# Performance work log

Measured on AMD Instinct MI355X. Metric: run time of the kernel, lower is better.

## Reference

```python
import jax, jax.numpy as jnp
import numpy as np
import math

B, S, H = 4, 1024, 1024
E, TOP_K, WINDOW = 4, 2, 64
CONFIGS = [(8, 'standard'), (12, 'standard'), (8, 'linear'), (8, 'local')]
PARAM_NAMES = ['Wq', 'bq', 'Wk', 'bk', 'Wv', 'bv', 'Wo', 'bo']


def setup_inputs() -> dict:
    key = jax.random.key(0)
    ks = jax.random.split(key, 2 + 8 * E)
    d = {}
    d['x'] = jax.random.normal(ks[0], (B, S, H), jnp.float32)
    d['Wg'] = jax.random.normal(ks[1], (H, E), jnp.float32) * 0.02
    i = 2
    for e, (nh, _) in enumerate(CONFIGS):
        hd = H // nh
        pd = nh * hd  # 1020 for nh=12, else 1024
        shapes = [(H, pd), (pd,), (H, pd), (pd,), (H, pd), (pd,), (pd, H), (H,)]
        for nm, shp in zip(PARAM_NAMES, shapes):
            d[f'e{e}_{nm}'] = jax.random.normal(ks[i], shp, jnp.float32) * 0.02
            i += 1
    d['attention_mask'] = jnp.ones((B, S), jnp.int32)
    return d


def _heads(y, nh, hd):
    b, s, _ = y.shape
    return y.reshape(b, s, nh, hd).transpose(0, 2, 1, 3)  # [b, nh, s, hd]


def _attention_expert(x, mask, Wq, bq, Wk, bk, Wv, bv, Wo, bo, nh, atype):
    b, s, _ = x.shape
    hd = Wq.shape[1] // nh
    scale = math.sqrt(hd)
    q = _heads(x @ Wq + bq, nh, hd)
    k = _heads(x @ Wk + bk, nh, hd)
    v = _heads(x @ Wv + bv, nh, hd)
    if atype == 'linear':
        # kernel-trick linear attention; original ignores attention_mask here
        q = jax.nn.elu(q) + 1.0
        k = jax.nn.elu(k) + 1.0
        kv = jnp.einsum('bhsd,bhse->bhde', k, v)
        num = jnp.einsum('bhqd,bhde->bhqe', q, kv)
        den = jnp.einsum('bhqd,bhd->bhq', q, k.sum(axis=2)) + 1e-6
        out = num / den[..., None]
    else:
        scores = jnp.einsum('bhqd,bhkd->bhqk', q, k) / scale
        if atype == 'local':
            idx = jnp.arange(s)
            dist = idx[None, :] - idx[:, None]  # j - i
            local_mask = jnp.abs(dist) <= WINDOW // 2
            scores = jnp.where(local_mask[None, None], scores, -jnp.inf)
        scores = jnp.where(mask[:, None, None, :] == 0, -jnp.inf, scores)
        probs = jax.nn.softmax(scores, axis=-1)
        probs = jnp.where(jnp.isnan(probs), 0.0, probs)  # nan_to_num(nan=0)
        out = jnp.einsum('bhqk,bhkd->bhqd', probs, v)
    out = out.transpose(0, 2, 1, 3).reshape(b, s, -1)
    return out @ Wo + bo


def _forward(x, Wg, eparams, attention_mask):
    b, s, h = x.shape
    # TopKGating (eval mode: no noise). logits -> top_k -> softmax over selected
    logits = x.reshape(-1, h) @ Wg  # [b*s, E]
    top_vals, top_idx = jax.lax.top_k(logits, TOP_K)
    gate_w = jax.nn.softmax(top_vals, axis=-1).reshape(b, s, TOP_K)
    sel = top_idx.reshape(b, s, TOP_K)
    outs = jnp.stack([
        _attention_expert(x, attention_mask, *eparams[e], CONFIGS[e][0], CONFIGS[e][1])
        for e in range(E)
    ], axis=0)  # [E, b, s, h]
    perm = outs.transpose(1, 2, 0, 3)  # [b, s, E, h]
    selected = jnp.take_along_axis(perm, sel[..., None], axis=2)  # [b, s, K, h]
    return (selected * gate_w[..., None]).sum(axis=2)


def reference(x, Wg,
              e0_Wq, e0_bq, e0_Wk, e0_bk, e0_Wv, e0_bv, e0_Wo, e0_bo,
              e1_Wq, e1_bq, e1_Wk, e1_bk, e1_Wv, e1_bv, e1_Wo, e1_bo,
              e2_Wq, e2_bq, e2_Wk, e2_bk, e2_Wv, e2_bv, e2_Wo, e2_bo,
              e3_Wq, e3_bq, e3_Wk, e3_bk, e3_Wv, e3_bv, e3_Wo, e3_bo,
              attention_mask):
    eparams = [
        (e0_Wq, e0_bq, e0_Wk, e0_bk, e0_Wv, e0_bv, e0_Wo, e0_bo),
        (e1_Wq, e1_bq, e1_Wk, e1_bk, e1_Wv, e1_bv, e1_Wo, e1_bo),
        (e2_Wq, e2_bq, e2_Wk, e2_bk, e2_Wv, e2_bv, e2_Wo, e2_bo),
        (e3_Wq, e3_bq, e3_Wk, e3_bk, e3_Wv, e3_bv, e3_Wo, e3_bo),
    ]
    return _forward(x, Wg, eparams, attention_mask)
```

## Files before the change

### kernel.cpp

```cpp
#include <hip/hip_runtime.h>
#include <cmath>

#define B_ 4
#define S_ 1024
#define H_ 1024

typedef short bf16x8 __attribute__((ext_vector_type(8)));
typedef float f32x4 __attribute__((ext_vector_type(4)));
typedef _Float16 half4 __attribute__((ext_vector_type(4)));

__device__ __forceinline__ unsigned short f2bf(float f) {
  unsigned u = __float_as_uint(f);
  u += 0x7fff + ((u >> 16) & 1);
  return (unsigned short)(u >> 16);
}
__device__ __forceinline__ float bf2f(unsigned short h) {
  return __uint_as_float(((unsigned)h) << 16);
}
__device__ __forceinline__ void gld16(const void* g, void* l) {
  __builtin_amdgcn_global_load_lds(
      (const __attribute__((address_space(1))) unsigned int*)g,
      (__attribute__((address_space(3))) unsigned int*)l, 16, 0, 0);
}

__global__ __launch_bounds__(64) void gate_kernel(
    const float* __restrict__ x, const float* __restrict__ Wg,
    float* __restrict__ gw) {
  int t = blockIdx.x;
  int lane = threadIdx.x;
  const float* xr = x + (size_t)t * H_;
  float a0 = 0.f, a1 = 0.f, a2 = 0.f, a3 = 0.f;
  for (int h = lane; h < H_; h += 64) {
    float xv = xr[h];
    const float* wr = Wg + h * 4;
    a0 += xv * wr[0]; a1 += xv * wr[1]; a2 += xv * wr[2]; a3 += xv * wr[3];
  }
  for (int off = 32; off > 0; off >>= 1) {
    a0 += __shfl_down(a0, off);
    a1 += __shfl_down(a1, off);
    a2 += __shfl_down(a2, off);
    a3 += __shfl_down(a3, off);
  }
  if (lane == 0) {
    float v[4] = {a0, a1, a2, a3};
    int i0 = 0; float b0 = v[0];
    for (int e = 1; e < 4; ++e) if (v[e] > b0) { b0 = v[e]; i0 = e; }
    int i1 = -1; float b1 = -INFINITY;
    for (int e = 0; e < 4; ++e) { if (e == i0) continue; if (v[e] > b1) { b1 = v[e]; i1 = e; } }
    float e1v = expf(b1 - b0);
    float w0 = 1.f / (1.f + e1v);
    float w1 = e1v / (1.f + e1v);
    float o[4] = {0.f, 0.f, 0.f, 0.f};
    o[i0] = w0; o[i1] = w1;
    float* g = gw + t * 4;
    g[0] = o[0]; g[1] = o[1]; g[2] = o[2]; g[3] = o[3];
  }
}

__global__ __launch_bounds__(64) void gate_conv_kernel(
    const float* __restrict__ x, const float* __restrict__ Wg,
    float* __restrict__ gw, unsigned short* __restrict__ xb) {
  int t = blockIdx.x;
  int lane = threadIdx.x;
  const float* xr = x + (size_t)t * H_;
  unsigned short* xbr = xb + (size_t)t * H_;
  float a0 = 0.f, a1 = 0.f, a2 = 0.f, a3 = 0.f;
  for (int h = lane; h < H_; h += 64) {
    float xv = xr[h];
    xbr[h] = f2bf(xv);
    const float* wr = Wg + h * 4;
    a0 += xv * wr[0]; a1 += xv * wr[1]; a2 += xv * wr[2]; a3 += xv * wr[3];
  }
  for (int off = 32; off > 0; off >>= 1) {
    a0 += __shfl_down(a0, off);
    a1 += __shfl_down(a1, off);
    a2 += __shfl_down(a2, off);
    a3 += __shfl_down(a3, off);
  }
  if (lane == 0) {
    float v[4] = {a0, a1, a2, a3};
    int i0 = 0; float b0 = v[0];
    for (int e = 1; e < 4; ++e) if (v[e] > b0) { b0 = v[e]; i0 = e; }
    int i1 = -1; float b1 = -INFINITY;
    for (int e = 0; e < 4; ++e) { if (e == i0) continue; if (v[e] > b1) { b1 = v[e]; i1 = e; } }
    float e1v = expf(b1 - b0);
    float w0 = 1.f / (1.f + e1v);
    float w1 = e1v / (1.f + e1v);
    float o[4] = {0.f, 0.f, 0.f, 0.f};
    o[i0] = w0; o[i1] = w1;
    float* g = gw + t * 4;
    g[0] = o[0]; g[1] = o[1]; g[2] = o[2]; g[3] = o[3];
  }
}

__global__ __launch_bounds__(256) void conv_kernel(
    const float* __restrict__ src, unsigned short* __restrict__ dst,
    int nsrc, int ldsrc) {
  int idx = blockIdx.x * 256 + threadIdx.x;
  int m = idx >> 10, c = idx & 1023;
  dst[idx] = (c < nsrc) ? f2bf(src[(size_t)m * ldsrc + c]) : (unsigned short)0;
}

__global__ __launch_bounds__(256) void wtrans4_kernel(
    const float* __restrict__ s0, const float* __restrict__ s1,
    const float* __restrict__ s2, const float* __restrict__ s3,
    unsigned short* __restrict__ d0, unsigned short* __restrict__ d1,
    unsigned short* __restrict__ d2, unsigned short* __restrict__ d3, int pd) {
  __shared__ float tile[32][33];
  int z = blockIdx.z;
  const float* src = (z == 0) ? s0 : (z == 1) ? s1 : (z == 2) ? s2 : s3;
  unsigned short* dst = (z == 0) ? d0 : (z == 1) ? d1 : (z == 2) ? d2 : d3;
  int ksrc = (z < 3) ? 1024 : pd;
  int nsrc = (z < 3) ? pd : 1024;
  int ldsrc = (z < 3) ? pd : 1024;
  int k0 = blockIdx.x * 32, n0 = blockIdx.y * 32;
  int tx = threadIdx.x & 31, ty = threadIdx.x >> 5;
  for (int i = 0; i < 32; i += 8) {
    int k = k0 + ty + i, n = n0 + tx;
    tile[ty + i][tx] = (k < ksrc && n < nsrc) ? src[(size_t)k * ldsrc + n] : 0.f;
  }
  __syncthreads();
  for (int i = 0; i < 32; i += 8) {
    int n = n0 + ty + i, k = k0 + tx;
    dst[(size_t)n * 1024 + k] = f2bf(tile[tx][ty + i]);
  }
}

struct W16 {
  const float* src[16];
  unsigned short* dst[16];
  int pd[4];
};
__global__ __launch_bounds__(256) void wtrans16_kernel(W16 p) {
  __shared__ float tile[32][33];
  int z = blockIdx.z;
  int e = z >> 2, m = z & 3;
  const float* src = p.src[z];
  unsigned short* dst = p.dst[z];
  int pd = p.pd[e];
  int ksrc = (m < 3) ? 1024 : pd;
  int nsrc = (m < 3) ? pd : 1024;
  int ldsrc = (m < 3) ? pd : 1024;
  int k0 = blockIdx.x * 32, n0 = blockIdx.y * 32;
  int tx = threadIdx.x & 31, ty = threadIdx.x >> 5;
  for (int i = 0; i < 32; i += 8) {
    int k = k0 + ty + i, n = n0 + tx;
    tile[ty + i][tx] = (k < ksrc && n < nsrc) ? src[(size_t)k * ldsrc + n] : 0.f;
  }
  __syncthreads();
  for (int i = 0; i < 32; i += 8) {
    int n = n0 + ty + i, k = k0 + tx;
    dst[(size_t)n * 1024 + k] = f2bf(tile[tx][ty + i]);
  }
}

__global__ __launch_bounds__(256) void gemm_mfma(
    const unsigned short* __restrict__ A, const unsigned short* __restrict__ Bt,
    const float* __restrict__ b0, const float* __restrict__ b1,
    const float* __restrict__ b2, void* __restrict__ Cv, int ldc,
    int nact, int elu_ncut, int out_bf16, int mode,
    const float* __restrict__ gw, int expert, int remap,
    int qs_ncut, float qscale) {
  constexpr int K = 1024;
  __shared__ __align__(16) unsigned short As[128 * 32];
  __shared__ __align__(16) unsigned short Bs[128 * 32];
  int tid = threadIdx.x, wave = tid >> 6, lane = tid & 63;
  int quad = lane >> 4, lrow = lane & 15;
  int rw = (wave >> 1) * 64, cw = (wave & 1) * 64;
  int m0 = blockIdx.y * 128, n0 = blockIdx.x * 128;
  int srow = wave * 32 + (lane >> 2);
  int scol = (lane & 3) * 8;
  const unsigned short* gA = A + (size_t)(m0 + srow) * K + scol;
  const unsigned short* gB = Bt + (size_t)(n0 + srow) * K + scol;
  unsigned short* lA = &As[wave * 1024];
  unsigned short* lB = &Bs[wave * 1024];
  f32x4 acc[4][4];
#pragma unroll
  for (int mt = 0; mt < 4; ++mt)
#pragma unroll
    for (int nt = 0; nt < 4; ++nt) acc[mt][nt] = (f32x4){0.f, 0.f, 0.f, 0.f};

  for (int k0 = 0; k0 < K; k0 += 32) {
    gld16(gA + k0, lA);
    gld16(gA + 16 * K + k0, lA + 512);
    gld16(gB + k0, lB);
    gld16(gB + 16 * K + k0, lB + 512);
    __syncthreads();
    bf16x8 af[4], bfr[4];
#pragma unroll
    for (int t = 0; t < 4; ++t) {
      af[t]  = *(const bf16x8*)&As[(rw + t * 16 + lrow) * 32 + quad * 8];
      bfr[t] = *(const bf16x8*)&Bs[(cw + t * 16 + lrow) * 32 + quad * 8];
    }
#pragma unroll
    for (int mt = 0; mt < 4; ++mt)
#pragma unroll
      for (int nt = 0; nt < 4; ++nt)
        acc[mt][nt] = __builtin_amdgcn_mfma_f32_16x16x32_bf16(
            af[mt], bfr[nt], acc[mt][nt], 0, 0, 0);
    __syncthreads();
  }
#pragma unroll
  for (int nt = 0; nt < 4; ++nt) {
    int n = n0 + cw + nt * 16 + lrow;
    int slice = n >> 10, noff = n & 1023;
    if (noff >= nact) continue;
    const float* bp = (slice == 0) ? b0 : (slice == 1) ? b1 : b2;
    float bias = bp[noff];
    bool do_elu = n < elu_ncut;
    bool do_qs = n < qs_ncut;
    int col = n;
    if (remap) {
      int head = (noff * 12337) >> 20;
      col = slice * 1152 + head * 96 + (noff - head * 85);
    }
#pragma unroll
    for (int mt = 0; mt < 4; ++mt) {
      int mb = m0 + rw + mt * 16 + quad * 4;
#pragma unroll
      for (int r = 0; r < 4; ++r) {
        int m = mb + r;
        float val = acc[mt][nt][r] + bias;
        if (do_elu) val = (val > 0.f) ? val + 1.f : expf(val);
        if (do_qs) val *= qscale;
        size_t ci = (size_t)m * ldc + col;
        if (out_bf16) {
          ((unsigned short*)Cv)[ci] = f2bf(val);
        } else {
          float* C = (float*)Cv;
          if (mode == 0) C[ci] = val;
          else {
            float g = gw[m * 4 + expert];
            if (mode == 1) C[ci] = g * val;
            else           C[ci] += g * val;
          }
        }
      }
    }
  }
}

struct QkvP {
  const unsigned short* Bt[4];
  const float* bq[4];
  const float* bk[4];
  const float* bv[4];
  unsigned short* C[4];
  int ldc[4];
  int nact[4];
  int elu_ncut[4];
  int remap[4];
  int qs_ncut[4];
  float qscale[4];
};
__global__ __launch_bounds__(256) void gemm_qkv4(
    const unsigned short* __restrict__ A, QkvP p) {
  constexpr int K = 1024;
  __shared__ __align__(16) unsigned short As[2 * 128 * 32];
  __shared__ __align__(16) unsigned short Bs[2 * 128 * 32];
  int e = blockIdx.z;
  const unsigned short* Bt = p.Bt[e];
  unsigned short* Cv = p.C[e];
  int ldc = p.ldc[e], nact = p.nact[e], elu_ncut = p.elu_ncut[e];
  int remap = p.remap[e], qs_ncut = p.qs_ncut[e];
  float qscale = p.qscale[e];
  int tid = threadIdx.x, wave = tid >> 6, lane = tid & 63;
  int quad = lane >> 4, lrow = lane & 15;
  int rw = (wave >> 1) * 64, cw = (wave & 1) * 64;
  int m0 = blockIdx.y * 128, n0 = blockIdx.x * 128;
  int srow = wave * 32 + (lane >> 2);
  int scol = (lane & 3) * 8;
  const unsigned short* gA = A + (size_t)(m0 + srow) * K + scol;
  const unsigned short* gB = Bt + (size_t)(n0 + srow) * K + scol;
  unsigned short* lA = &As[wave * 1024];
  unsigned short* lB = &Bs[wave * 1024];
  f32x4 acc[4][4];
#pragma unroll
  for (int mt = 0; mt < 4; ++mt)
#pragma unroll
    for (int nt = 0; nt < 4; ++nt) acc[mt][nt] = (f32x4){0.f, 0.f, 0.f, 0.f};

  for (int k0 = 0; k0 < K; k0 += 64) {
    gld16(gA + k0, lA);
    gld16(gA + 16 * K + k0, lA + 512);
    gld16(gA + k0 + 32, lA + 4096);
    gld16(gA + 16 * K + k0 + 32, lA + 4096 + 512);
    gld16(gB + k0, lB);
    gld16(gB + 16 * K + k0, lB + 512);
    gld16(gB + k0 + 32, lB + 4096);
    gld16(gB + 16 * K + k0 + 32, lB + 4096 + 512);
    __syncthreads();
#pragma unroll
    for (int kk = 0; kk < 2; ++kk) {
      const unsigned short* Ap = As + kk * 4096;
      const unsigned short* Bp = Bs + kk * 4096;
      bf16x8 af[4], bfr[4];
#pragma unroll
      for (int t = 0; t < 4; ++t) {
        af[t]  = *(const bf16x8*)&Ap[(rw + t * 16 + lrow) * 32 + quad * 8];
        bfr[t] = *(const bf16x8*)&Bp[(cw + t * 16 + lrow) * 32 + quad * 8];
      }
#pragma unroll
      for (int mt = 0; mt < 4; ++mt)
#pragma unroll
        for (int nt = 0; nt < 4; ++nt)
          acc[mt][nt] = __builtin_amdgcn_mfma_f32_16x16x32_bf16(
              af[mt], bfr[nt], acc[mt][nt], 0, 0, 0);
    }
    __syncthreads();
  }
#pragma unroll
  for (int nt = 0; nt < 4; ++nt) {
    int n = n0 + cw + nt * 16 + lrow;
    int slice = n >> 10, noff = n & 1023;
    if (noff >= nact) continue;
    const float* bp = (slice == 0) ? p.bq[e] : (slice == 1) ? p.bk[e] : p.bv[e];
    float bias = bp[noff];
    bool do_elu = n < elu_ncut;
    bool do_qs = n < qs_ncut;
    int col = n;
    if (remap) {
      int head = (noff * 12337) >> 20;
      col = slice * 1152 + head * 96 + (noff - head * 85);
    }
#pragma unroll
    for (int mt = 0; mt < 4; ++mt) {
      int mb = m0 + rw + mt * 16 + quad * 4;
#pragma unroll
      for (int r = 0; r < 4; ++r) {
        int m = mb + r;
        float val = acc[mt][nt][r] + bias;
        if (do_elu) val = (val > 0.f) ? val + 1.f : expf(val);
        if (do_qs) val *= qscale;
        Cv[(size_t)m * ldc + col] = f2bf(val);
      }
    }
  }
}

struct OutP {
  const unsigned short* A[4];
  const unsigned short* B[4];
  const float* bias[4];
};

__global__ __launch_bounds__(256) void gemm_out4(
    OutP p, const float* __restrict__ gw, float* __restrict__ part) {
  constexpr int K = 1024;
  __shared__ __align__(16) unsigned short As[2 * 128 * 32];
  __shared__ __align__(16) unsigned short Bs[2 * 128 * 32];
  int e = blockIdx.z;
  const unsigned short* A = p.A[e];
  const unsigned short* Bt = p.B[e];
  const float* bp = p.bias[e];
  float* C = part + (size_t)e * (4096ull * 1024ull);
  int tid = threadIdx.x, wave = tid >> 6, lane = tid & 63;
  int quad = lane >> 4, lrow = lane & 15;
  int rw = (wave >> 1) * 64, cw = (wave & 1) * 64;
  int m0 = blockIdx.y * 128, n0 = blockIdx.x * 128;
  int srow = wave * 32 + (lane >> 2);
  int scol = (lane & 3) * 8;
  const unsigned short* gA = A + (size_t)(m0 + srow) * K + scol;
  const unsigned short* gB = Bt + (size_t)(n0 + srow) * K + scol;
  unsigned short* lA = &As[wave * 1024];
  unsigned short* lB = &Bs[wave * 1024];
  f32x4 acc[4][4];
#pragma unroll
  for (int mt = 0; mt < 4; ++mt)
#pragma unroll
    for (int nt = 0; nt < 4; ++nt) acc[mt][nt] = (f32x4){0.f, 0.f, 0.f, 0.f};

  for (int k0 = 0; k0 < K; k0 += 64) {
    gld16(gA + k0, lA);
    gld16(gA + 16 * K + k0, lA + 512);
    gld16(gA + k0 + 32, lA + 4096);
    gld16(gA + 16 * K + k0 + 32, lA + 4096 + 512);
    gld16(gB + k0, lB);
    gld16(gB + 16 * K + k0, lB + 512);
    gld16(gB + k0 + 32, lB + 4096);
    gld16(gB + 16 * K + k0 + 32, lB + 4096 + 512);
    __syncthreads();
#pragma unroll
    for (int kk = 0; kk < 2; ++kk) {
      const unsigned short* Ap = As + kk * 4096;
      const unsigned short* Bp = Bs + kk * 4096;
      bf16x8 af[4], bfr[4];
#pragma unroll
      for (int t = 0; t < 4; ++t) {
        af[t]  = *(const bf16x8*)&Ap[(rw + t * 16 + lrow) * 32 + quad * 8];
        bfr[t] = *(const bf16x8*)&Bp[(cw + t * 16 + lrow) * 32 + quad * 8];
      }
#pragma unroll
      for (int mt = 0; mt < 4; ++mt)
#pragma unroll
        for (int nt = 0; nt < 4; ++nt)
          acc[mt][nt] = __builtin_amdgcn_mfma_f32_16x16x32_bf16(
              af[mt], bfr[nt], acc[mt][nt], 0, 0, 0);
    }
    __syncthreads();
  }
#pragma unroll
  for (int nt = 0; nt < 4; ++nt) {
    int n = n0 + cw + nt * 16 + lrow;
    float bias = bp[n];
#pragma unroll
    for (int mt = 0; mt < 4; ++mt) {
      int mb = m0 + rw + mt * 16 + quad * 4;
#pragma unroll
      for (int r = 0; r < 4; ++r) {
        int m = mb + r;
        float g = gw[m * 4 + e];
        C[(size_t)m * 1024 + n] = g * (acc[mt][nt][r] + bias);
      }
    }
  }
}

__global__ __launch_bounds__(256) void reduce4(
    const float* __restrict__ part, float* __restrict__ out) {
  constexpr size_t N = 4096ull * 1024ull;
  size_t idx = ((size_t)blockIdx.x * 256 + threadIdx.x) * 4;
  f32x4 a0 = *(const f32x4*)(part + idx);
  f32x4 a1 = *(const f32x4*)(part + idx + N);
  f32x4 a2 = *(const f32x4*)(part + idx + 2 * N);
  f32x4 a3 = *(const f32x4*)(part + idx + 3 * N);
  f32x4 s;
#pragma unroll
  for (int j = 0; j < 4; ++j) {
    float t = a0[j];
    t += a1[j]; t += a2[j]; t += a3[j];
    s[j] = t;
  }
  *(f32x4*)(out + idx) = s;
}

__global__ __launch_bounds__(256) void padzero(
    unsigned short* __restrict__ qkv1, unsigned short* __restrict__ aob1) {
  int idx = blockIdx.x * 256 + threadIdx.x;
  int m = idx / 396, r = idx % 396;
  int slice = r / 132, r2 = r % 132;
  int head = r2 / 11, c = 85 + r2 % 11;
  qkv1[(size_t)m * 3456 + slice * 1152 + head * 96 + c] = 0;
  if (idx < 4096 * 4) {
    int mm = idx >> 2, cc = 1020 + (idx & 3);
    aob1[(size_t)mm * 1024 + cc] = 0;
  }
}

template <int HD, bool LOCAL>
__device__ __forceinline__ void attn_body(
    char* smem,
    const unsigned short* __restrict__ q, const unsigned short* __restrict__ k,
    const unsigned short* __restrict__ v, const int* __restrict__ amask,
    unsigned short* __restrict__ ao, int ldq, int h) {
  constexpr int HDP = (HD + 31) & ~31;
  constexpr int DCH = HDP / 32;
  constexpr int NDT = HDP / 16;
  constexpr int NCH = HDP / 8;
  constexpr int QT = 256, KT = 64;
  constexpr int KLD = HDP + 8;
  constexpr int VLD = KT + 4;
  constexpr int W2 = 32;
  constexpr int KSZ = KT * KLD;
  constexpr int VSZ = HDP * VLD;
  unsigned short* Ks = (unsigned short*)smem;
  _Float16* Vt = (_Float16*)(smem + 2 * KSZ * 2);
  unsigned long long* amq =
      (unsigned long long*)(smem + 2 * KSZ * 2 + 2 * VSZ * 2);
  int tid = threadIdx.x, wave = tid >> 6, lane = tid & 63;
  int quad = lane >> 4, l15 = lane & 15;
  int q0 = blockIdx.x * QT, b = blockIdx.z;
  size_t baseq = ((size_t)b * S_) * ldq + (size_t)h * HDP;
  size_t baseo = ((size_t)b * S_) * H_ + (size_t)h * HD;

  {
    unsigned long long bb0 = __ballot(amask[b * S_ + wave * 128 + lane] != 0);
    unsigned long long bb1 = __ballot(amask[b * S_ + wave * 128 + 64 + lane] != 0);
    if (lane == 0) { amq[wave * 2] = bb0; amq[wave * 2 + 1] = bb1; }
  }

  int qrow[2];
  bf16x8 qf[2][DCH];
#pragma unroll
  for (int g = 0; g < 2; ++g) {
    qrow[g] = q0 + wave * 32 + g * 16 + l15;
#pragma unroll
    for (int c = 0; c < DCH; ++c)
#pragma unroll
      for (int j = 0; j < 8; ++j) {
        int d = c * 32 + quad * 8 + j;
        qf[g][c][j] =
            (d < HD) ? (short)q[baseq + (size_t)qrow[g] * ldq + d] : (short)0;
      }
  }

  int jlo = 0, jhi = S_;
  if (LOCAL) {
    jlo = q0 - W2; if (jlo < 0) jlo = 0; jlo &= ~(KT - 1);
    jhi = q0 + QT + W2; if (jhi > S_) jhi = S_;
  }

  int skey = tid & 63, sc8a = tid >> 6, sc8b = 8 + (tid >> 6);
  bool sactb = sc8b < NCH;
  const unsigned short* kg = k + baseq + (size_t)skey * ldq;
  const unsigned short* vg = v + baseq + (size_t)skey * ldq;
  bf16x8 kra = {}, krb = {}, vra = {}, vrb = {};
  {
    size_t o = (size_t)jlo * ldq;
    kra = *(const bf16x8*)(kg + o + sc8a * 8);
    vra = *(const bf16x8*)(vg + o + sc8a * 8);
    if (sactb) {
      krb = *(const bf16x8*)(kg + o + sc8b * 8);
      vrb = *(const bf16x8*)(vg + o + sc8b * 8);
    }
  }

  {
    *(bf16x8*)&Ks[skey * KLD + sc8a * 8] = kra;
#pragma unroll
    for (int j = 0; j < 8; ++j)
      Vt[(sc8a * 8 + j) * VLD + skey] = (_Float16)bf2f((unsigned short)vra[j]);
    if (sactb) {
      *(bf16x8*)&Ks[skey * KLD + sc8b * 8] = krb;
#pragma unroll
      for (int j = 0; j < 8; ++j)
        Vt[(sc8b * 8 + j) * VLD + skey] = (_Float16)bf2f((unsigned short)vrb[j]);
    }
  }
  int cur = 0;
  __syncthreads();

  float m_run[2] = {-1e30f, -1e30f}, l_run[2] = {0.f, 0.f};
  f32x4 accd[2][NDT];
#pragma unroll
  for (int g = 0; g < 2; ++g)
#pragma unroll
    for (int dt = 0; dt < NDT; ++dt) accd[g][dt] = (f32x4){0.f, 0.f, 0.f, 0.f};

  for (int j0 = jlo; j0 < jhi; j0 += KT) {
    int jn = j0 + KT;
    if (jn < jhi) {
      size_t o = (size_t)jn * ldq;
      kra = *(const bf16x8*)(kg + o + sc8a * 8);
      vra = *(const bf16x8*)(vg + o + sc8a * 8);
      if (sactb) {
        krb = *(const bf16x8*)(kg + o + sc8b * 8);
        vrb = *(const bf16x8*)(vg + o + sc8b * 8);
      }
    }
    const unsigned short* KsR = Ks + cur * KSZ;
    const _Float16* VtR = Vt + cur * VSZ;
    f32x4 sf[2][4];
#pragma unroll
    for (int kt = 0; kt < 4; ++kt) {
      sf[0][kt] = (f32x4){0.f, 0.f, 0.f, 0.f};
      sf[1][kt] = (f32x4){0.f, 0.f, 0.f, 0.f};
#pragma unroll
      for (int c = 0; c < DCH; ++c) {
        bf16x8 kf = *(const bf16x8*)&KsR[(kt * 16 + l15) * KLD + c * 32 + quad * 8];
        sf[0][kt] = __builtin_amdgcn_mfma_f32_16x16x32_bf16(kf, qf[0][c], sf[0][kt], 0, 0, 0);
        sf[1][kt] = __builtin_amdgcn_mfma_f32_16x16x32_bf16(kf, qf[1][c], sf[1][kt], 0, 0, 0);
      }
    }
    unsigned long long mb = amq[j0 >> 6];
    unsigned mw[2] = {(unsigned)mb, (unsigned)(mb >> 32)};
    float pvv[2][4][4];
    float mx[2] = {-1e30f, -1e30f};
#pragma unroll
    for (int kt = 0; kt < 4; ++kt) {
      unsigned word = mw[kt >> 1];
      int sh = (kt & 1) * 16 + quad * 4;
#pragma unroll
      for (int r = 0; r < 4; ++r) {
        bool okm = (word >> (sh + r)) & 1;
#pragma unroll
        for (int g = 0; g < 2; ++g) {
          bool ok = okm;
          if (LOCAL) {
            int dj = (j0 + kt * 16 + quad * 4 + r) - qrow[g];
            ok = ok && (dj <= W2) && (dj >= -W2);
          }
          float s = ok ? sf[g][kt][r] : -1e30f;
          pvv[g][kt][r] = s;
          mx[g] = fmaxf(mx[g], s);
        }
      }
    }
    half4 pf[2][4];
    float aR[2][4];
#pragma unroll
    for (int g = 0; g < 2; ++g) {
      float mxg = fmaxf(mx[g], __shfl_xor(mx[g], 16));
      mxg = fmaxf(mxg, __shfl_xor(mxg, 32));
      float m_new = fmaxf(m_run[g], mxg);
      float psum = 0.f;
#pragma unroll
      for (int kt = 0; kt < 4; ++kt)
#pragma unroll
        for (int r = 0; r < 4; ++r) {
          float s = pvv[g][kt][r];
          float p = (s > -1e29f) ? __builtin_amdgcn_exp2f(s - m_new) : 0.f;
          pvv[g][kt][r] = p;
          psum += p;
        }
      psum += __shfl_xor(psum, 16);
      psum += __shfl_xor(psum, 32);
      float alpha = __builtin_amdgcn_exp2f(m_run[g] - m_new);
      m_run[g] = m_new;
      l_run[g] = l_run[g] * alpha + psum;
#pragma unroll
      for (int r = 0; r < 4; ++r)
        aR[g][r] = __shfl(alpha, (lane & 48) | (quad * 4 + r));
#pragma unroll
      for (int dt = 0; dt < NDT; ++dt)
#pragma unroll
        for (int r = 0; r < 4; ++r) accd[g][dt][r] *= aR[g][r];
#pragma unroll
      for (int kt = 0; kt < 4; ++kt)
#pragma unroll
        for (int r = 0; r < 4; ++r) pf[g][kt][r] = (_Float16)pvv[g][kt][r];
    }
    if (jn < jhi) {
      unsigned short* KsW = Ks + (cur ^ 1) * KSZ;
      _Float16* VtW = Vt + (cur ^ 1) * VSZ;
      *(bf16x8*)&KsW[skey * KLD + sc8a * 8] = kra;
#pragma unroll
      for (int j = 0; j < 8; ++j)
        VtW[(sc8a * 8 + j) * VLD + skey] = (_Float16)bf2f((unsigned short)vra[j]);
      if (sactb) {
        *(bf16x8*)&KsW[skey * KLD + sc8b * 8] = krb;
#pragma unroll
        for (int j = 0; j < 8; ++j)
          VtW[(sc8b * 8 + j) * VLD + skey] = (_Float16)bf2f((unsigned short)vrb[j]);
      }
    }
#pragma unroll
    for (int dt = 0; dt < NDT; ++dt)
#pragma unroll
      for (int kt = 0; kt < 4; ++kt) {
        half4 vf = *(const half4*)&VtR[(dt * 16 + l15) * VLD + kt * 16 + quad * 4];
        accd[0][dt] = __builtin_amdgcn_mfma_f32_16x16x16f16(pf[0][kt], vf, accd[0][dt], 0, 0, 0);
        accd[1][dt] = __builtin_amdgcn_mfma_f32_16x16x16f16(pf[1][kt], vf, accd[1][dt], 0, 0, 0);
      }
    __syncthreads();
    cur ^= 1;
  }
#pragma unroll
  for (int g = 0; g < 2; ++g) {
    float linv = (l_run[g] > 0.f) ? 1.f / l_run[g] : 0.f;
    float lR[4];
#pragma unroll
    for (int r = 0; r < 4; ++r)
      lR[r] = __shfl(linv, (lane & 48) | (quad * 4 + r));
#pragma unroll
    for (int dt = 0; dt < NDT; ++dt) {
      int d = dt * 16 + l15;
      if (d >= HD) continue;
#pragma unroll
      for (int r = 0; r < 4; ++r) {
        int row = q0 + wave * 32 + g * 16 + quad * 4 + r;
        ao[baseo + (size_t)row * H_ + d] = f2bf(accd[g][dt][r] * lR[r]);
      }
    }
  }
}

template <int HD, bool LOCAL>
__global__ __launch_bounds__(512) void attn_mfma3(
    const unsigned short* __restrict__ q, const unsigned short* __restrict__ k,
    const unsigned short* __restrict__ v, const int* __restrict__ amask,
    unsigned short* __restrict__ ao, int ldq) {
  constexpr int HDP = (HD + 31) & ~31;
  __shared__ __align__(16) char smem[2 * 64 * (HDP + 8) * 2 + 2 * HDP * 68 * 2 + 128];
  attn_body<HD, LOCAL>(smem, q, k, v, amask, ao, ldq, blockIdx.y);
}

#define NSPLIT 4
__device__ __forceinline__ void linkv_body(
    char* smemi, const unsigned short* __restrict__ k,
    const unsigned short* __restrict__ v, float* __restrict__ kvp,
    float* __restrict__ ksump, int ld, int h, int b, int split, int tid) {
  constexpr int HD = 128;
  constexpr int TLD = 34;
  unsigned short* Kt = (unsigned short*)smemi;
  unsigned short* Vt = Kt + HD * TLD;
  int bh = b * 8 + h;
  int wave = tid >> 6, lane = tid & 63;
  int quad = lane >> 4, l15 = lane & 15;
  int rw = (wave >> 1) * 64, cw = (wave & 1) * 64;
  size_t base = ((size_t)b * S_) * ld + (size_t)h * HD;
  int s_begin = split * (S_ / NSPLIT);

  f32x4 acc[4][4];
#pragma unroll
  for (int mt = 0; mt < 4; ++mt)
#pragma unroll
    for (int nt = 0; nt < 4; ++nt) acc[mt][nt] = (f32x4){0.f, 0.f, 0.f, 0.f};
  float ksacc = 0.f;
  int myd = tid & 127, half = tid >> 7;

  for (int c0 = 0; c0 < S_ / NSPLIT; c0 += 32) {
    for (int idx = tid; idx < 32 * HD; idx += 256) {
      int d = idx & 127, s = idx >> 7;
      size_t g = base + (size_t)(s_begin + c0 + s) * ld + d;
      Kt[d * TLD + s] = k[g];
      Vt[d * TLD + s] = v[g];
    }
    __syncthreads();
    bf16x8 af[4], bf[4];
#pragma unroll
    for (int t = 0; t < 4; ++t) {
      af[t] = *(const bf16x8*)&Vt[(rw + t * 16 + l15) * TLD + quad * 8];
      bf[t] = *(const bf16x8*)&Kt[(cw + t * 16 + l15) * TLD + quad * 8];
    }
#pragma unroll
    for (int mt = 0; mt < 4; ++mt)
#pragma unroll
      for (int nt = 0; nt < 4; ++nt)
        acc[mt][nt] = __builtin_amdgcn_mfma_f32_16x16x32_bf16(
            af[mt], bf[nt], acc[mt][nt], 0, 0, 0);
#pragma unroll
    for (int s = 0; s < 16; ++s)
      ksacc += bf2f(Kt[myd * TLD + half * 16 + s]);
    __syncthreads();
  }
  float* red = (float*)Kt;
  if (half == 1) red[myd] = ksacc;
  __syncthreads();
  if (half == 0)
    ksump[((size_t)split * 32 + bh) * HD + myd] = ksacc + red[myd];
  float* kvo = kvp + ((size_t)split * 32 + bh) * (HD * HD);
#pragma unroll
  for (int mt = 0; mt < 4; ++mt)
#pragma unroll
    for (int nt = 0; nt < 4; ++nt) {
      int dk = cw + nt * 16 + l15;
#pragma unroll
      for (int r = 0; r < 4; ++r) {
        int dv = rw + mt * 16 + quad * 4 + r;
        kvo[(size_t)dv * HD + dk] = acc[mt][nt][r];
      }
    }
}

__global__ __launch_bounds__(256) void linkv_mfma(
    const unsigned short* __restrict__ k, const unsigned short* __restrict__ v,
    float* __restrict__ kvp, float* __restrict__ ksump, int ld) {
  __shared__ __align__(16) char smemi[17408];
  linkv_body(smemi, k, v, kvp, ksump, ld, blockIdx.x, blockIdx.y, blockIdx.z,
             threadIdx.x);
}

__global__ __launch_bounds__(512) void attn_mega(
    const unsigned short* __restrict__ qkv0,
    const unsigned short* __restrict__ qkv1,
    const unsigned short* __restrict__ qkv2,
    const unsigned short* __restrict__ qkv3, const int* __restrict__ amask,
    unsigned short* __restrict__ ao0, unsigned short* __restrict__ ao1,
    unsigned short* __restrict__ ao3,
    float* __restrict__ kvp, float* __restrict__ ksump) {
  __shared__ __align__(16) char smem[69760];
  int y = blockIdx.y;
  if (y < 8)
    attn_body<128, false>(smem, qkv0, qkv0 + 1024, qkv0 + 2048, amask, ao0,
                          3072, y);
  else if (y < 20)
    attn_body<85, false>(smem, qkv1, qkv1 + 1152, qkv1 + 2304, amask, ao1,
                         3456, y - 8);
  else if (y < 28)
    attn_body<128, true>(smem, qkv3, qkv3 + 1024, qkv3 + 2048, amask, ao3,
                         3072, y - 20);
  else {
    int sub = threadIdx.x >> 8, stid = threadIdx.x & 255;
    int idx = (y - 28) * 8 + blockIdx.x * 2 + sub;
    linkv_body(smem + sub * 17408, qkv2 + 1024, qkv2 + 2048, kvp, ksump, 3072,
               idx & 7, blockIdx.z, idx >> 3, stid);
  }
}

__global__ __launch_bounds__(256) void linkv_reduce(
    const float* __restrict__ kvp, const float* __restrict__ ksump,
    unsigned short* __restrict__ kvb, float* __restrict__ ksum) {
  int idx = blockIdx.x * 256 + threadIdx.x;
  float s = 0.f;
#pragma unroll
  for (int p = 0; p < NSPLIT; ++p) s += kvp[(size_t)p * (32 * 128 * 128) + idx];
  kvb[idx] = f2bf(s);
  if (idx < 32 * 128) {
    float t = 0.f;
#pragma unroll
    for (int p = 0; p < NSPLIT; ++p) t += ksump[(size_t)p * (32 * 128) + idx];
    ksum[idx] = t;
  }
}

__global__ __launch_bounds__(256) void linattn_mfma(
    const unsigned short* __restrict__ q, const unsigned short* __restrict__ kvT,
    const float* __restrict__ ksum, unsigned short* __restrict__ ao, int ldq) {
  constexpr int KLD = 136;
  __shared__ __align__(16) unsigned short Ks[128 * KLD];
  __shared__ float ksL[128];
  int tid = threadIdx.x, wave = tid >> 6, lane = tid & 63;
  int quad = lane >> 4, l15 = lane & 15;
  int rw = (wave >> 1) * 64, cw = (wave & 1) * 64;
  int q0 = blockIdx.x * 128, h = blockIdx.y, b = blockIdx.z;
  int bh = b * 8 + h;
  size_t baseq = ((size_t)b * S_) * ldq + (size_t)h * 128;
  size_t baseo = ((size_t)b * S_) * H_ + (size_t)h * 128;
  const unsigned short* kvg = kvT + (size_t)bh * (128 * 128);
  for (int idx = tid; idx < 128 * 16; idx += 256) {
    int e = idx >> 4, c = idx & 15;
    *(bf16x8*)&Ks[e * KLD + c * 8] = *(const bf16x8*)&kvg[e * 128 + c * 8];
  }
  if (tid < 128) ksL[tid] = ksum[(size_t)bh * 128 + tid];
  bf16x8 qf[4][4];
#pragma unroll
  for (int mt = 0; mt < 4; ++mt) {
    const unsigned short* qr = q + baseq + (size_t)(q0 + rw + mt * 16 + l15) * ldq;
#pragma unroll
    for (int kc = 0; kc < 4; ++kc)
      qf[mt][kc] = *(const bf16x8*)&qr[kc * 32 + quad * 8];
  }
  __syncthreads();
  f32x4 acc[4][4];
#pragma unroll
  for (int mt = 0; mt < 4; ++mt)
#pragma unroll
    for (int nt = 0; nt < 4; ++nt) acc[mt][nt] = (f32x4){0.f, 0.f, 0.f, 0.f};
#pragma unroll
  for (int kc = 0; kc < 4; ++kc) {
    bf16x8 bf[4];
#pragma unroll
    for (int nt = 0; nt < 4; ++nt)
      bf[nt] = *(const bf16x8*)&Ks[(cw + nt * 16 + l15) * KLD + kc * 32 + quad * 8];
#pragma unroll
    for (int mt = 0; mt < 4; ++mt)
#pragma unroll
      for (int nt = 0; nt < 4; ++nt)
        acc[mt][nt] = __builtin_amdgcn_mfma_f32_16x16x32_bf16(
            qf[mt][kc], bf[nt], acc[mt][nt], 0, 0, 0);
  }
  float den[4];
#pragma unroll
  for (int mt = 0; mt < 4; ++mt) {
    float s = 0.f;
#pragma unroll
    for (int kc = 0; kc < 4; ++kc)
#pragma unroll
      for (int j = 0; j < 8; ++j)
        s += bf2f((unsigned short)qf[mt][kc][j]) * ksL[kc * 32 + quad * 8 + j];
    s += __shfl_xor(s, 16);
    s += __shfl_xor(s, 32);
    den[mt] = s;
  }
#pragma unroll
  for (int mt = 0; mt < 4; ++mt)
#pragma unroll
    for (int r = 0; r < 4; ++r) {
      float dv = __shfl(den[mt], (lane & 48) | (quad * 4 + r));
      float inv = 1.f / (dv + 1e-6f);
      int row = q0 + rw + mt * 16 + quad * 4 + r;
#pragma unroll
      for (int nt = 0; nt < 4; ++nt) {
        int col = cw + nt * 16 + l15;
        ao[baseo + (size_t)row * H_ + col] = f2bf(acc[mt][nt][r] * inv);
      }
    }
}

extern "C" void kernel_launch(void* const* d_in, const int* in_sizes, int n_in,
                              void* d_out, int out_size, void* d_ws, size_t ws_size,
                              hipStream_t stream) {
  const float* x = (const float*)d_in[0];
  const float* Wg = (const float*)d_in[1];
  const int* amask = (const int*)d_in[34];
  float* out = (float*)d_out;
  char* ws = (char*)d_ws;
  const size_t MiB = 1ull << 20;
  const int nhs[4] = {8, 12, 8, 8};
  const float LOG2E = 1.4426950408889634f;

  if (ws_size >= 157 * MiB) {
    float* gw = (float*)ws;
    float* ksum = (float*)(ws + (64ull << 10));
    unsigned short* kvb = (unsigned short*)(ws + 1 * MiB);
    unsigned short* xb = (unsigned short*)(ws + 4 * MiB);
    float* kvp = (float*)(ws + 4 * MiB);
    float* ksump = (float*)(ws + 12 * MiB);
    unsigned short* woT[4];
    for (int e = 0; e < 4; ++e)
      woT[e] = (unsigned short*)(ws + (18 + 2 * e) * MiB);
    const size_t qkvOff[4] = {26 * MiB, 50 * MiB, 77 * MiB, 101 * MiB};
    unsigned short* qkvE[4];
    for (int e = 0; e < 4; ++e) qkvE[e] = (unsigned short*)(ws + qkvOff[e]);
    float* part = (float*)(ws + 26 * MiB);
    unsigned short* aobE[4];
    for (int e = 0; e < 4; ++e)
      aobE[e] = (unsigned short*)(ws + (125 + 8 * e) * MiB);
    unsigned short* qkvT4 = (unsigned short*)(ws + 125 * MiB);

    gate_conv_kernel<<<4096, 64, 0, stream>>>(x, Wg, gw, xb);

    W16 w;
    for (int e = 0; e < 4; ++e) {
      w.pd[e] = nhs[e] * (H_ / nhs[e]);
      for (int m = 0; m < 3; ++m) {
        w.src[e * 4 + m] = (const float*)d_in[2 + 8 * e + 2 * m];
        w.dst[e * 4 + m] = qkvT4 + (size_t)(e * 3 + m) * (1 << 20);
      }
      w.src[e * 4 + 3] = (const float*)d_in[2 + 8 * e + 6];
      w.dst[e * 4 + 3] = woT[e];
    }
    wtrans16_kernel<<<dim3(32, 32, 16), 256, 0, stream>>>(w);

    QkvP qp;
    for (int e = 0; e < 4; ++e) {
      int hd = H_ / nhs[e];
      int pd = nhs[e] * hd;
      qp.Bt[e] = qkvT4 + (size_t)(e * 3) * (1 << 20);
      qp.bq[e] = (const float*)d_in[2 + 8 * e + 1];
      qp.bk[e] = (const float*)d_in[2 + 8 * e + 3];
      qp.bv[e] = (const float*)d_in[2 + 8 * e + 5];
      qp.C[e] = qkvE[e];
      qp.ldc[e] = (e == 1) ? 3456 : 3072;
      qp.nact[e] = (pd == 1020) ? 1020 : 1024;
      qp.elu_ncut[e] = (e == 2) ? 2048 : 0;
      qp.remap[e] = (e == 1) ? 1 : 0;
      qp.qs_ncut[e] = (e == 2) ? 0 : 1024;
      qp.qscale[e] = LOG2E / sqrtf((float)hd);
    }
    gemm_qkv4<<<dim3(24, 32, 4), 256, 0, stream>>>(xb, qp);

    padzero<<<6336, 256, 0, stream>>>(qkvE[1], aobE[1]);

    attn_mega<<<dim3(S_ / 256, 32, B_), 512, 0, stream>>>(
        qkvE[0], qkvE[1], qkvE[2], qkvE[3], amask, aobE[0], aobE[1], aobE[3],
        kvp, ksump);

    linkv_reduce<<<(32 * 128 * 128) / 256, 256, 0, stream>>>(kvp, ksump, kvb, ksum);
    linattn_mfma<<<dim3(S_ / 128, 8, B_), 256, 0, stream>>>(
        qkvE[2], kvb, ksum, aobE[2], 3072);

    OutP p;
    for (int e = 0; e < 4; ++e) {
      p.A[e] = aobE[e];
      p.B[e] = woT[e];
      p.bias[e] = (const float*)d_in[2 + 8 * e + 7];
    }
    gemm_out4<<<dim3(8, 32, 4), 256, 0, stream>>>(p, gw, part);
    reduce4<<<4096, 256, 0, stream>>>(part, out);
    return;
  }

  float* gw            = (float*)(ws + 0);
  unsigned short* kvb  = (unsigned short*)(ws + (1ull << 20));
  float* ksum          = (float*)(ws + (3ull << 20) + (1ull << 19));
  unsigned short* xb   = (unsigned short*)(ws + (4ull << 20));
  unsigned short* qkvT = (unsigned short*)(ws + (12ull << 20));
  unsigned short* woT  = (unsigned short*)(ws + (18ull << 20));
  unsigned short* qkv  = (unsigned short*)(ws + (20ull << 20));
  unsigned short* aob  = (unsigned short*)(ws + (49ull << 20));
  float* kvp           = (float*)(ws + (57ull << 20));
  float* ksump         = (float*)(ws + (73ull << 20));

  conv_kernel<<<16384, 256, 0, stream>>>(x, xb, 1024, 1024);
  gate_kernel<<<4096, 64, 0, stream>>>(x, Wg, gw);

  for (int e = 0; e < 4; ++e) {
    const float* Wq = (const float*)d_in[2 + 8 * e + 0];
    const float* bq = (const float*)d_in[2 + 8 * e + 1];
    const float* Wk = (const float*)d_in[2 + 8 * e + 2];
    const float* bk = (const float*)d_in[2 + 8 * e + 3];
    const float* Wv = (const float*)d_in[2 + 8 * e + 4];
    const float* bv = (const float*)d_in[2 + 8 * e + 5];
    const float* Wo = (const float*)d_in[2 + 8 * e + 6];
    const float* bo = (const float*)d_in[2 + 8 * e + 7];
    int nh = nhs[e];
    int hd = H_ / nh;
    int pd = nh * hd;
    int ldqkv = (e == 1) ? 3456 : 3072;
    int qs_ncut = (e == 2) ? 0 : 1024;
    float qscale = LOG2E / sqrtf((float)hd);

    wtrans4_kernel<<<dim3(32, 32, 4), 256, 0, stream>>>(
        Wq, Wk, Wv, Wo, qkvT, qkvT + (1 << 20), qkvT + (2 << 20), woT, pd);

    gemm_mfma<<<dim3(24, 32), 256, 0, stream>>>(
        xb, qkvT, bq, bk, bv, qkv, ldqkv,
        (pd == 1020) ? 1020 : 1024, (e == 2) ? 2048 : 0, 1, 0, nullptr, 0,
        (e == 1) ? 1 : 0, qs_ncut, qscale);

    if (e == 2) {
      const unsigned short* qb = qkv;
      const unsigned short* kb = qkv + 1024;
      const unsigned short* vb = qkv + 2048;
      linkv_mfma<<<dim3(8, B_, NSPLIT), 256, 0, stream>>>(kb, vb, kvp, ksump, 3072);
      linkv_reduce<<<(32 * 128 * 128) / 256, 256, 0, stream>>>(kvp, ksump, kvb, ksum);
      linattn_mfma<<<dim3(S_ / 128, 8, B_), 256, 0, stream>>>(qb, kvb, ksum, aob, 3072);
    } else if (e == 1) {
      attn_mfma3<85, false><<<dim3(S_ / 256, 12, B_), 512, 0, stream>>>(
          qkv, qkv + 1152, qkv + 2304, amask, aob, 3456);
    } else if (e == 3) {
      attn_mfma3<128, true><<<dim3(S_ / 256, 8, B_), 512, 0, stream>>>(
          qkv, qkv + 1024, qkv + 2048, amask, aob, 3072);
    } else {
      attn_mfma3<128, false><<<dim3(S_ / 256, 8, B_), 512, 0, stream>>>(
          qkv, qkv + 1024, qkv + 2048, amask, aob, 3072);
    }

    gemm_mfma<<<dim3(8, 32), 256, 0, stream>>>(
        aob, woT, bo, bo, bo, out, 1024, 1024, 0, 0, (e == 0) ? 1 : 2, gw, e, 0,
        0, 1.0f);
  }
}
```

Baseline: 527.8 us.

## Rewrite QKV and output GEMMs as 256x256 double-buffered tiles with swizzled LDS

```diff
diff --git a/kernel.cpp b/kernel.cpp
--- a/kernel.cpp
+++ b/kernel.cpp
@@ -240,6 +240,86 @@
   }
 }
 
+__device__ __forceinline__ void stage_half(
+    const unsigned short* __restrict__ G, int grow0, int kbase,
+    unsigned short* lhalf, int wave, int lane) {
+#pragma unroll
+  for (int j = 0; j < 2; ++j) {
+    int t = j * 512 + wave * 64 + lane;
+    int rl = t >> 3;
+    int cs = (t & 7) * 8;
+    int c0 = cs ^ (((rl >> 2) & 1) << 4);
+    gld16(G + (size_t)(grow0 + rl) * 1024 + kbase + c0,
+          lhalf + (size_t)(j * 512 + wave * 64) * 8);
+  }
+}
+
+__device__ __forceinline__ void gemm256_core(
+    const unsigned short* __restrict__ A, const unsigned short* __restrict__ Bt,
+    int m0, int n0, unsigned short* As, unsigned short* Bs,
+    f32x4 (&acc)[8][4]) {
+  int tid = threadIdx.x;
+  int wave = tid >> 6, lane = tid & 63;
+  int quad = lane >> 4, l15 = lane & 15;
+  int wr = wave >> 2, wc = wave & 3;
+#pragma unroll
+  for (int mr = 0; mr < 8; ++mr)
+#pragma unroll
+    for (int nr = 0; nr < 4; ++nr) acc[mr][nr] = (f32x4){0.f, 0.f, 0.f, 0.f};
+  stage_half(A, m0, 0, As, wave, lane);
+  stage_half(A, m0 + 128, 0, As + 8192, wave, lane);
+  stage_half(Bt, n0, 0, Bs, wave, lane);
+  stage_half(Bt, n0 + 128, 0, Bs + 8192, wave, lane);
+  __syncthreads();
+  int cur = 0;
+  for (int t = 0; t < 16; ++t) {
+    const unsigned short* Ar = As + cur * 16384;
+    const unsigned short* Br = Bs + cur * 16384;
+    unsigned short* Awr = As + (cur ^ 1) * 16384;
+    unsigned short* Bwr = Bs + (cur ^ 1) * 16384;
+    int kb = (t + 1) * 64;
+    bool more = (t + 1 < 16);
+    bf16x8 bfr[4];
+#pragma unroll
+    for (int p = 0; p < 4; ++p) {
+      const int ks = p >> 1, mh = (p & 1) * 4;
+      bf16x8 af[4];
+#pragma unroll
+      for (int i = 0; i < 4; ++i) {
+        int row = wr * 128 + (mh + i) * 16 + l15;
+        int c = ks * 32 + quad * 8;
+        af[i] = *(const bf16x8*)&Ar[row * 64 + (c ^ (((row >> 2) & 1) << 4))];
+      }
+      if ((p & 1) == 0) {
+#pragma unroll
+        for (int i = 0; i < 4; ++i) {
+          int row = wc * 64 + i * 16 + l15;
+          int c = ks * 32 + quad * 8;
+          bfr[i] = *(const bf16x8*)&Br[row * 64 + (c ^ (((row >> 2) & 1) << 4))];
+        }
+      }
+      if (more) {
+        if (p == 0) stage_half(A, m0, kb, Awr, wave, lane);
+        else if (p == 1) stage_half(A, m0 + 128, kb, Awr + 8192, wave, lane);
+        else if (p == 2) stage_half(Bt, n0, kb, Bwr, wave, lane);
+        else stage_half(Bt, n0 + 128, kb, Bwr + 8192, wave, lane);
+      }
+      __builtin_amdgcn_s_barrier();
+      __builtin_amdgcn_s_setprio(1);
+#pragma unroll
+      for (int i = 0; i < 4; ++i)
+#pragma unroll
+        for (int jn = 0; jn < 4; ++jn)
+          acc[mh + i][jn] = __builtin_amdgcn_mfma_f32_16x16x32_bf16(
+              af[i], bfr[jn], acc[mh + i][jn], 0, 0, 0);
+      __builtin_amdgcn_s_setprio(0);
+      __builtin_amdgcn_s_barrier();
+    }
+    __syncthreads();
+    cur ^= 1;
+  }
+}
+
 struct QkvP {
   const unsigned short* Bt[4];
   const float* bq[4];
@@ -253,65 +333,26 @@
   int qs_ncut[4];
   float qscale[4];
 };
-__global__ __launch_bounds__(256) void gemm_qkv4(
+__global__ __launch_bounds__(512, 1) void gemm_qkv4_v2(
     const unsigned short* __restrict__ A, QkvP p) {
-  constexpr int K = 1024;
-  __shared__ __align__(16) unsigned short As[2 * 128 * 32];
-  __shared__ __align__(16) unsigned short Bs[2 * 128 * 32];
+  __shared__ __align__(16) unsigned short As[2 * 256 * 64];
+  __shared__ __align__(16) unsigned short Bs[2 * 256 * 64];
   int e = blockIdx.z;
-  const unsigned short* Bt = p.Bt[e];
+  int flat = blockIdx.y * 12 + blockIdx.x;
+  int swz = (flat & 7) * 24 + (flat >> 3);
+  int m0 = (swz / 12) * 256, n0 = (swz % 12) * 256;
+  f32x4 acc[8][4];
+  gemm256_core(A, p.Bt[e], m0, n0, As, Bs, acc);
+  int nact = p.nact[e], elu_ncut = p.elu_ncut[e], remap = p.remap[e];
+  int qs_ncut = p.qs_ncut[e], ldc = p.ldc[e];
+  float qscale = p.qscale[e];
   unsigned short* Cv = p.C[e];
-  int ldc = p.ldc[e], nact = p.nact[e], elu_ncut = p.elu_ncut[e];
-  int remap = p.remap[e], qs_ncut = p.qs_ncut[e];
-  float qscale = p.qscale[e];
   int tid = threadIdx.x, wave = tid >> 6, lane = tid & 63;
-  int quad = lane >> 4, lrow = lane & 15;
-  int rw = (wave >> 1) * 64, cw = (wave & 1) * 64;
-  int m0 = blockIdx.y * 128, n0 = blockIdx.x * 128;
-  int srow = wave * 32 + (lane >> 2);
-  int scol = (lane & 3) * 8;
-  const unsigned short* gA = A + (size_t)(m0 + srow) * K + scol;
-  const unsigned short* gB = Bt + (size_t)(n0 + srow) * K + scol;
-  unsigned short* lA = &As[wave * 1024];
-  unsigned short* lB = &Bs[wave * 1024];
-  f32x4 acc[4][4];
-#pragma unroll
-  for (int mt = 0; mt < 4; ++mt)
-#pragma unroll
-    for (int nt = 0; nt < 4; ++nt) acc[mt][nt] = (f32x4){0.f, 0.f, 0.f, 0.f};
-
-  for (int k0 = 0; k0 < K; k0 += 64) {
-    gld16(gA + k0, lA);
-    gld16(gA + 16 * K + k0, lA + 512);
-    gld16(gA + k0 + 32, lA + 4096);
-    gld16(gA + 16 * K + k0 + 32, lA + 4096 + 512);
-    gld16(gB + k0, lB);
-    gld16(gB + 16 * K + k0, lB + 512);
-    gld16(gB + k0 + 32, lB + 4096);
-    gld16(gB + 16 * K + k0 + 32, lB + 4096 + 512);
-    __syncthreads();
-#pragma unroll
-    for (int kk = 0; kk < 2; ++kk) {
-      const unsigned short* Ap = As + kk * 4096;
-      const unsigned short* Bp = Bs + kk * 4096;
-      bf16x8 af[4], bfr[4];
-#pragma unroll
-      for (int t = 0; t < 4; ++t) {
-        af[t]  = *(const bf16x8*)&Ap[(rw + t * 16 + lrow) * 32 + quad * 8];
-        bfr[t] = *(const bf16x8*)&Bp[(cw + t * 16 + lrow) * 32 + quad * 8];
-      }
-#pragma unroll
-      for (int mt = 0; mt < 4; ++mt)
-#pragma unroll
-        for (int nt = 0; nt < 4; ++nt)
-          acc[mt][nt] = __builtin_amdgcn_mfma_f32_16x16x32_bf16(
-              af[mt], bfr[nt], acc[mt][nt], 0, 0, 0);
-    }
-    __syncthreads();
-  }
-#pragma unroll
-  for (int nt = 0; nt < 4; ++nt) {
-    int n = n0 + cw + nt * 16 + lrow;
+  int quad = lane >> 4, l15 = lane & 15;
+  int wr = wave >> 2, wc = wave & 3;
+#pragma unroll
+  for (int nr = 0; nr < 4; ++nr) {
+    int n = n0 + wc * 64 + nr * 16 + l15;
     int slice = n >> 10, noff = n & 1023;
     if (noff >= nact) continue;
     const float* bp = (slice == 0) ? p.bq[e] : (slice == 1) ? p.bk[e] : p.bv[e];
@@ -324,12 +365,12 @@
       col = slice * 1152 + head * 96 + (noff - head * 85);
     }
 #pragma unroll
-    for (int mt = 0; mt < 4; ++mt) {
-      int mb = m0 + rw + mt * 16 + quad * 4;
+    for (int mr = 0; mr < 8; ++mr) {
+      int mb = m0 + wr * 128 + mr * 16 + quad * 4;
 #pragma unroll
       for (int r = 0; r < 4; ++r) {
         int m = mb + r;
-        float val = acc[mt][nt][r] + bias;
+        float val = acc[mr][nr][r] + bias;
         if (do_elu) val = (val > 0.f) ? val + 1.f : expf(val);
         if (do_qs) val *= qscale;
         Cv[(size_t)m * ldc + col] = f2bf(val);
@@ -343,74 +384,33 @@
   const unsigned short* B[4];
   const float* bias[4];
 };
-
-__global__ __launch_bounds__(256) void gemm_out4(
+__global__ __launch_bounds__(512, 1) void gemm_out4_v2(
     OutP p, const float* __restrict__ gw, float* __restrict__ part) {
-  constexpr int K = 1024;
-  __shared__ __align__(16) unsigned short As[2 * 128 * 32];
-  __shared__ __align__(16) unsigned short Bs[2 * 128 * 32];
+  __shared__ __align__(16) unsigned short As[2 * 256 * 64];
+  __shared__ __align__(16) unsigned short Bs[2 * 256 * 64];
   int e = blockIdx.z;
-  const unsigned short* A = p.A[e];
-  const unsigned short* Bt = p.B[e];
+  int flat = blockIdx.y * 4 + blockIdx.x;
+  int swz = (flat & 7) * 8 + (flat >> 3);
+  int m0 = (swz / 4) * 256, n0 = (swz % 4) * 256;
+  f32x4 acc[8][4];
+  gemm256_core(p.A[e], p.B[e], m0, n0, As, Bs, acc);
   const float* bp = p.bias[e];
   float* C = part + (size_t)e * (4096ull * 1024ull);
   int tid = threadIdx.x, wave = tid >> 6, lane = tid & 63;
-  int quad = lane >> 4, lrow = lane & 15;
-  int rw = (wave >> 1) * 64, cw = (wave & 1) * 64;
-  int m0 = blockIdx.y * 128, n0 = blockIdx.x * 128;
-  int srow = wave * 32 + (lane >> 2);
-  int scol = (lane & 3) * 8;
-  const unsigned short* gA = A + (size_t)(m0 + srow) * K + scol;
-  const unsigned short* gB = Bt + (size_t)(n0 + srow) * K + scol;
-  unsigned short* lA = &As[wave * 1024];
-  unsigned short* lB = &Bs[wave * 1024];
-  f32x4 acc[4][4];
-#pragma unroll
-  for (int mt = 0; mt < 4; ++mt)
-#pragma unroll
-    for (int nt = 0; nt < 4; ++nt) acc[mt][nt] = (f32x4){0.f, 0.f, 0.f, 0.f};
-
-  for (int k0 = 0; k0 < K; k0 += 64) {
-    gld16(gA + k0, lA);
-    gld16(gA + 16 * K + k0, lA + 512);
-    gld16(gA + k0 + 32, lA + 4096);
-    gld16(gA + 16 * K + k0 + 32, lA + 4096 + 512);
-    gld16(gB + k0, lB);
-    gld16(gB + 16 * K + k0, lB + 512);
-    gld16(gB + k0 + 32, lB + 4096);
-    gld16(gB + 16 * K + k0 + 32, lB + 4096 + 512);
-    __syncthreads();
-#pragma unroll
-    for (int kk = 0; kk < 2; ++kk) {
-      const unsigned short* Ap = As + kk * 4096;
-      const unsigned short* Bp = Bs + kk * 4096;
-      bf16x8 af[4], bfr[4];
-#pragma unroll
-      for (int t = 0; t < 4; ++t) {
-        af[t]  = *(const bf16x8*)&Ap[(rw + t * 16 + lrow) * 32 + quad * 8];
-        bfr[t] = *(const bf16x8*)&Bp[(cw + t * 16 + lrow) * 32 + quad * 8];
-      }
-#pragma unroll
-      for (int mt = 0; mt < 4; ++mt)
-#pragma unroll
-        for (int nt = 0; nt < 4; ++nt)
-          acc[mt][nt] = __builtin_amdgcn_mfma_f32_16x16x32_bf16(
-              af[mt], bfr[nt], acc[mt][nt], 0, 0, 0);
-    }
-    __syncthreads();
-  }
-#pragma unroll
-  for (int nt = 0; nt < 4; ++nt) {
-    int n = n0 + cw + nt * 16 + lrow;
+  int quad = lane >> 4, l15 = lane & 15;
+  int wr = wave >> 2, wc = wave & 3;
+#pragma unroll
+  for (int nr = 0; nr < 4; ++nr) {
+    int n = n0 + wc * 64 + nr * 16 + l15;
     float bias = bp[n];
 #pragma unroll
-    for (int mt = 0; mt < 4; ++mt) {
-      int mb = m0 + rw + mt * 16 + quad * 4;
+    for (int mr = 0; mr < 8; ++mr) {
+      int mb = m0 + wr * 128 + mr * 16 + quad * 4;
 #pragma unroll
       for (int r = 0; r < 4; ++r) {
         int m = mb + r;
         float g = gw[m * 4 + e];
-        C[(size_t)m * 1024 + n] = g * (acc[mt][nt][r] + bias);
+        C[(size_t)m * 1024 + n] = g * (acc[mr][nr][r] + bias);
       }
     }
   }
@@ -929,7 +929,7 @@
       qp.qs_ncut[e] = (e == 2) ? 0 : 1024;
       qp.qscale[e] = LOG2E / sqrtf((float)hd);
     }
-    gemm_qkv4<<<dim3(24, 32, 4), 256, 0, stream>>>(xb, qp);
+    gemm_qkv4_v2<<<dim3(12, 16, 4), 512, 0, stream>>>(xb, qp);
 
     padzero<<<6336, 256, 0, stream>>>(qkvE[1], aobE[1]);
 
@@ -947,7 +947,7 @@
       p.B[e] = woT[e];
       p.bias[e] = (const float*)d_in[2 + 8 * e + 7];
     }
-    gemm_out4<<<dim3(8, 32, 4), 256, 0, stream>>>(p, gw, part);
+    gemm_out4_v2<<<dim3(4, 16, 4), 512, 0, stream>>>(p, gw, part);
     reduce4<<<4096, 256, 0, stream>>>(part, out);
     return;
   }
```

Measured after the change: 524.6 us. Within noise of the previous version (-0.6%).
